# Optimization experiments

Hardware: AMD Instinct MI355X
Metric: run time of the kernel (lower is better)

The kernel has to match this reference:

```python
import jax, jax.numpy as jnp
import numpy as np

N_NODES = 100000
N_EDGES = 600000
D = 128          # input_dim
H = 256          # hidden_dim


def setup_inputs() -> dict:
    key = jax.random.key(0)
    k_emb, k_edge, k_w1, k_w2 = jax.random.split(key, 4)
    emd_all = jax.random.normal(k_emb, (N_NODES, D), dtype=jnp.float32)
    edge_index = jax.random.randint(k_edge, (N_EDGES, 2), 0, N_NODES, dtype=jnp.int32)
    # Linear(2*D, H) and Linear(H, 1); scale like torch default init ~ 1/sqrt(fan_in)
    W1 = jax.random.normal(k_w1, (2 * D, H), dtype=jnp.float32) / np.sqrt(2 * D)
    b1 = jnp.zeros((H,), dtype=jnp.float32)
    W2 = jax.random.normal(k_w2, (H, 1), dtype=jnp.float32) / np.sqrt(H)
    b2 = jnp.zeros((1,), dtype=jnp.float32)
    return {"emd_all": emd_all, "edge_index": edge_index,
            "W1": W1, "b1": b1, "W2": W2, "b2": b2}


def reference(emd_all, edge_index, W1, b1, W2, b2):
    # Gather source / destination node embeddings and concatenate: [E, 2*D]
    src = emd_all[edge_index[:, 0]]
    dst = emd_all[edge_index[:, 1]]
    edge_embeds = jnp.concatenate([src, dst], axis=-1)
    # 2-layer MLP classifier + sigmoid: [E, 1]
    h = jax.nn.relu(edge_embeds @ W1 + b1)
    logits = h @ W2 + b2
    link_predictions = jax.nn.sigmoid(logits)
    return link_predictions
```

## Files before the change

### kernel.cpp

```cpp
#include <hip/hip_runtime.h>
#include <hip/hip_bf16.h>

#define N_EDGES_C 600000
#define D_C 128

typedef __attribute__((ext_vector_type(8))) short short8;
typedef __attribute__((ext_vector_type(4))) float f32x4;

__device__ inline unsigned short f2bf(float f) {
    unsigned int u = __builtin_bit_cast(unsigned int, f);
    u += 0x7FFF + ((u >> 16) & 1);
    return (unsigned short)(u >> 16);
}

__global__ void prep_w1f(const float* __restrict__ W1, unsigned short* __restrict__ w1f) {
    int o = blockIdx.x * 256 + threadIdx.x;
    int j    = o & 7;
    int lane = (o >> 3) & 63;
    int kk   = (o >> 9) & 7;
    int nf   = o >> 12;
    int k = kk * 32 + (lane >> 4) * 8 + j;
    int n = nf * 16 + (lane & 15);
    w1f[o] = f2bf(W1[k * 256 + n]);
}

__global__ __launch_bounds__(256, 4) void edge_mlp(
    const float* __restrict__ emd,
    const int* __restrict__ eidx,
    const unsigned short* __restrict__ w1f,
    const float* __restrict__ b1,
    const float* __restrict__ W2,
    const float* __restrict__ b2,
    float* __restrict__ out)
{
    extern __shared__ unsigned char smem[];
    float* partial = (float*)(smem + 64 * 512);

    const int e0 = blockIdx.x * 64;
    const int t = threadIdx.x;

    #pragma unroll
    for (int p = 0; p < 16; ++p) {
        int c   = p * 256 + t;
        int row = c >> 6;
        int cb  = c & 63;
        int idx = eidx[(e0 + row) * 2 + (cb >> 5)];
        const float4 v = *reinterpret_cast<const float4*>(emd + (size_t)idx * D_C + (cb & 31) * 4);
        ushort4 pk;
        pk.x = f2bf(v.x); pk.y = f2bf(v.y); pk.z = f2bf(v.z); pk.w = f2bf(v.w);
        int boff = (row * 512 + cb * 8) ^ ((row & 7) << 4);
        *reinterpret_cast<ushort4*>(smem + boff) = pk;
    }
    __syncthreads();

    const int lane = t & 63;
    const int wv   = t >> 6;
    const int l15  = lane & 15;
    const int lg   = lane >> 4;

    f32x4 acc[4][4];
    #pragma unroll
    for (int m = 0; m < 4; ++m)
        #pragma unroll
        for (int n4 = 0; n4 < 4; ++n4) acc[m][n4] = (f32x4){0.f, 0.f, 0.f, 0.f};

    #pragma unroll
    for (int kk = 0; kk < 8; ++kk) {
        short8 a[4];
        #pragma unroll
        for (int m = 0; m < 4; ++m) {
            int r = m * 16 + l15;
            a[m] = *reinterpret_cast<const short8*>(
                smem + ((r * 512 + kk * 64 + lg * 16) ^ ((r & 7) << 4)));
        }
        #pragma unroll
        for (int n4 = 0; n4 < 4; ++n4) {
            int nf = wv * 4 + n4;
            short8 b = *reinterpret_cast<const short8*>(w1f + ((nf * 8 + kk) * 64 + lane) * 8);
            #pragma unroll
            for (int m = 0; m < 4; ++m)
                acc[m][n4] = __builtin_amdgcn_mfma_f32_16x16x32_bf16(a[m], b, acc[m][n4], 0, 0, 0);
        }
    }

    float pr[4][4];
    #pragma unroll
    for (int m = 0; m < 4; ++m)
        #pragma unroll
        for (int g = 0; g < 4; ++g) pr[m][g] = 0.f;

    #pragma unroll
    for (int n4 = 0; n4 < 4; ++n4) {
        int n = wv * 64 + n4 * 16 + l15;
        float b1v = b1[n];
        float w2v = W2[n];
        #pragma unroll
        for (int m = 0; m < 4; ++m)
            #pragma unroll
            for (int g = 0; g < 4; ++g) {
                float h = acc[m][n4][g] + b1v;
                h = h > 0.f ? h : 0.f;
                pr[m][g] += h * w2v;
            }
    }

    #pragma unroll
    for (int msk = 8; msk >= 1; msk >>= 1) {
        #pragma unroll
        for (int m = 0; m < 4; ++m)
            #pragma unroll
            for (int g = 0; g < 4; ++g)
                pr[m][g] += __shfl_xor(pr[m][g], msk, 64);
    }

    if (l15 == 0) {
        #pragma unroll
        for (int m = 0; m < 4; ++m)
            #pragma unroll
            for (int g = 0; g < 4; ++g)
                partial[wv * 64 + m * 16 + lg * 4 + g] = pr[m][g];
    }
    __syncthreads();

    if (t < 64) {
        float s = partial[t] + partial[64 + t] + partial[128 + t] + partial[192 + t] + b2[0];
        out[e0 + t] = 1.0f / (1.0f + __expf(-s));
    }
}

extern "C" void kernel_launch(void* const* d_in, const int* in_sizes, int n_in,
                              void* d_out, int out_size, void* d_ws, size_t ws_size,
                              hipStream_t stream) {
    const float* emd  = (const float*)d_in[0];
    const int*   eidx = (const int*)d_in[1];
    const float* W1   = (const float*)d_in[2];
    const float* b1   = (const float*)d_in[3];
    const float* W2   = (const float*)d_in[4];
    const float* b2   = (const float*)d_in[5];
    float* out = (float*)d_out;
    unsigned short* w1f = (unsigned short*)d_ws;

    prep_w1f<<<256, 256, 0, stream>>>(W1, w1f);

    const int nblocks = N_EDGES_C / 64;
    const size_t lds_bytes = 64 * 512 + 4 * 64 * sizeof(float);
    edge_mlp<<<nblocks, 256, lds_bytes, stream>>>(emd, eidx, w1f, b1, W2, b2, out);
}
```

Baseline: 135.1 us.

## Store gathered embeddings in MFMA fragment order in LDS and reuse the buffer for partials

Each thread now owns one edge row and loads its src and dst index pair as a single int2. It writes the bf16-converted features straight into a layout that matches the MFMA A-fragment, so the GEMM reads are contiguous per lane and need no XOR swizzle. LDS becomes a static 32KB array, and the partial-sum buffer reuses it after an extra barrier, which removes the extra 1KB. The launch_bounds occupancy hint is also dropped. The risks are a change in global load coalescing pattern (16 strided rows per wave) and possible LDS write bank conflicts.

```diff
diff --git a/kernel.cpp b/kernel.cpp
--- a/kernel.cpp
+++ b/kernel.cpp
@@ -13,6 +13,10 @@
     return (unsigned short)(u >> 16);
 }
 
+__device__ inline unsigned int pk2bf(float lo, float hi) {
+    return (unsigned int)f2bf(lo) | ((unsigned int)f2bf(hi) << 16);
+}
+
 __global__ void prep_w1f(const float* __restrict__ W1, unsigned short* __restrict__ w1f) {
     int o = blockIdx.x * 256 + threadIdx.x;
     int j    = o & 7;
@@ -24,7 +28,7 @@
     w1f[o] = f2bf(W1[k * 256 + n]);
 }
 
-__global__ __launch_bounds__(256, 4) void edge_mlp(
+__global__ __launch_bounds__(256) void edge_mlp(
     const float* __restrict__ emd,
     const int* __restrict__ eidx,
     const unsigned short* __restrict__ w1f,
@@ -33,30 +37,34 @@
     const float* __restrict__ b2,
     float* __restrict__ out)
 {
-    extern __shared__ unsigned char smem[];
-    float* partial = (float*)(smem + 64 * 512);
+    __shared__ unsigned char smem[32768];
+
+    const int t    = threadIdx.x;
+    const int lane = t & 63;
+    const int wv   = t >> 6;
+    const int rr   = lane & 15;
+    const int lg   = lane >> 4;
 
     const int e0 = blockIdx.x * 64;
-    const int t = threadIdx.x;
 
-    #pragma unroll
-    for (int p = 0; p < 16; ++p) {
-        int c   = p * 256 + t;
-        int row = c >> 6;
-        int cb  = c & 63;
-        int idx = eidx[(e0 + row) * 2 + (cb >> 5)];
-        const float4 v = *reinterpret_cast<const float4*>(emd + (size_t)idx * D_C + (cb & 31) * 4);
-        ushort4 pk;
-        pk.x = f2bf(v.x); pk.y = f2bf(v.y); pk.z = f2bf(v.z); pk.w = f2bf(v.w);
-        int boff = (row * 512 + cb * 8) ^ ((row & 7) << 4);
-        *reinterpret_cast<ushort4*>(smem + boff) = pk;
+    {
+        const int row = wv * 16 + rr;
+        const int2 e2 = *reinterpret_cast<const int2*>(eidx + (size_t)(e0 + row) * 2);
+        const float* ps = emd + (size_t)e2.x * D_C + lg * 4;
+        const float* pd = emd + (size_t)e2.y * D_C + lg * 4;
+        unsigned char* sw = smem + (wv * 8192 + (lg >> 1) * 256 + rr * 16 + (lg & 1) * 8);
+
+        #pragma unroll
+        for (int it = 0; it < 16; ++it) {
+            const float* p = (it < 8) ? ps : pd;
+            const float4 v = *reinterpret_cast<const float4*>(p + (it & 7) * 16);
+            uint2 pk;
+            pk.x = pk2bf(v.x, v.y);
+            pk.y = pk2bf(v.z, v.w);
+            *reinterpret_cast<uint2*>(sw + it * 512) = pk;
+        }
     }
     __syncthreads();
-
-    const int lane = t & 63;
-    const int wv   = t >> 6;
-    const int l15  = lane & 15;
-    const int lg   = lane >> 4;
 
     f32x4 acc[4][4];
     #pragma unroll
@@ -68,15 +76,12 @@
     for (int kk = 0; kk < 8; ++kk) {
         short8 a[4];
         #pragma unroll
-        for (int m = 0; m < 4; ++m) {
-            int r = m * 16 + l15;
-            a[m] = *reinterpret_cast<const short8*>(
-                smem + ((r * 512 + kk * 64 + lg * 16) ^ ((r & 7) << 4)));
-        }
+        for (int m = 0; m < 4; ++m)
+            a[m] = *reinterpret_cast<const short8*>(smem + (m * 8 + kk) * 1024 + lane * 16);
         #pragma unroll
         for (int n4 = 0; n4 < 4; ++n4) {
-            int nf = wv * 4 + n4;
-            short8 b = *reinterpret_cast<const short8*>(w1f + ((nf * 8 + kk) * 64 + lane) * 8);
+            short8 b = *reinterpret_cast<const short8*>(
+                w1f + ((size_t)((wv * 4 + n4) * 8 + kk) * 64 + lane) * 8);
             #pragma unroll
             for (int m = 0; m < 4; ++m)
                 acc[m][n4] = __builtin_amdgcn_mfma_f32_16x16x32_bf16(a[m], b, acc[m][n4], 0, 0, 0);
@@ -91,7 +96,7 @@
 
     #pragma unroll
     for (int n4 = 0; n4 < 4; ++n4) {
-        int n = wv * 64 + n4 * 16 + l15;
+        int n = wv * 64 + n4 * 16 + rr;
         float b1v = b1[n];
         float w2v = W2[n];
         #pragma unroll
@@ -113,7 +118,10 @@
                 pr[m][g] += __shfl_xor(pr[m][g], msk, 64);
     }
 
-    if (l15 == 0) {
+    __syncthreads();
+    float* partial = (float*)smem;
+
+    if (rr == 0) {
         #pragma unroll
         for (int m = 0; m < 4; ++m)
             #pragma unroll
@@ -143,6 +151,5 @@
     prep_w1f<<<256, 256, 0, stream>>>(W1, w1f);
 
     const int nblocks = N_EDGES_C / 64;
-    const size_t lds_bytes = 64 * 512 + 4 * 64 * sizeof(float);
-    edge_mlp<<<nblocks, 256, lds_bytes, stream>>>(emd, eidx, w1f, b1, W2, b2, out);
+    edge_mlp<<<nblocks, 256, 0, stream>>>(emd, eidx, w1f, b1, W2, b2, out);
 }
```

Result: slower. 164.8 us (+22.0%).
